# Kernel tuning notes

Measured on AMD Instinct MI355X. Metric: run time of the kernel, lower is better.

Reference implementation:

```python
import jax, jax.numpy as jnp
import numpy as np
from jax import lax

# Production-scale RPN detection-head config
B, FH, FW, NA = 8, 200, 200, 9      # batch, fmap h, fmap w, anchors/cell
H, W = 800, 800                      # image dims
N = FH * FW * NA                     # 360k anchors per image
NMS_THR = 0.7
MIN_SIZE = 1e-3


def _make_anchors():
    scales = np.array([32.0, 64.0, 128.0])
    ratios = np.array([0.5, 1.0, 2.0])
    ws = (scales[:, None] * np.sqrt(1.0 / ratios)[None, :]).reshape(-1)  # [NA]
    hs = (scales[:, None] * np.sqrt(ratios)[None, :]).reshape(-1)
    sy, sx = H / FH, W / FW
    cx = (np.arange(FW) + 0.5) * sx
    cy = (np.arange(FH) + 0.5) * sy
    cxg, cyg = np.meshgrid(cx, cy)                     # [FH,FW]
    cxg = cxg[..., None]; cyg = cyg[..., None]         # [FH,FW,1]
    a = np.stack([cxg - ws / 2, cyg - hs / 2, cxg + ws / 2, cyg + hs / 2], axis=-1)
    return jnp.asarray(a.reshape(-1, 4), jnp.float32)  # [N,4] xyxy


def setup_inputs() -> dict:
    key = jax.random.key(0)
    k1, k2 = jax.random.split(key)
    cls_logits = jax.random.normal(k1, (B, N, 1), jnp.float32)
    reg_deltas = jax.random.normal(k2, (B, N, 4), jnp.float32) * 0.1  # sane exp(dw)
    anchors = jnp.broadcast_to(_make_anchors()[None], (B, N, 4))
    return {
        "cls_logits": cls_logits,
        "reg_deltas": reg_deltas,
        "anchors": anchors,
        "keep_pre_nms": 1000,
        "keep_post_nms": 300,
    }


def _offsets2boxes(deltas, anchors):
    aw = anchors[:, 2] - anchors[:, 0]
    ah = anchors[:, 3] - anchors[:, 1]
    acx = anchors[:, 0] + 0.5 * aw
    acy = anchors[:, 1] + 0.5 * ah
    cx = deltas[:, 0] * aw + acx
    cy = deltas[:, 1] * ah + acy
    w = jnp.exp(deltas[:, 2]) * aw
    h = jnp.exp(deltas[:, 3]) * ah
    return jnp.stack([cx - 0.5 * w, cy - 0.5 * h, cx + 0.5 * w, cy + 0.5 * h], axis=-1)


def _iou_matrix(b):
    area = (b[:, 2] - b[:, 0]) * (b[:, 3] - b[:, 1])
    lt = jnp.maximum(b[:, None, :2], b[None, :, :2])
    rb = jnp.minimum(b[:, None, 2:], b[None, :, 2:])
    wh = jnp.clip(rb - lt, 0.0)
    inter = wh[..., 0] * wh[..., 1]
    return inter / (area[:, None] + area[None, :] - inter + 1e-9)


def _detect_one(logit, delta, anc, pre, post):
    scores = jax.nn.sigmoid(logit.reshape(-1))             # [N]
    boxes = _offsets2boxes(delta.reshape(-1, 4), anc)      # [N,4]
    s, idx = lax.top_k(scores, pre)                        # sorted desc
    b = boxes[idx]                                         # [pre,4]
    # clip to image
    b = jnp.stack([
        jnp.clip(b[:, 0], 0.0, W), jnp.clip(b[:, 1], 0.0, H),
        jnp.clip(b[:, 2], 0.0, W), jnp.clip(b[:, 3], 0.0, H)], axis=-1)
    valid = ((b[:, 2] - b[:, 0]) >= MIN_SIZE) & ((b[:, 3] - b[:, 1]) >= MIN_SIZE)
    # greedy NMS on score-sorted boxes (mask-based, fixed shapes)
    iou = _iou_matrix(lax.stop_gradient(b))                # [pre,pre]
    j = jnp.arange(pre)

    def body(keep, i):
        sup = (iou[i] > NMS_THR) & (j > i) & keep[i]
        return keep & ~sup, None

    keep, _ = lax.scan(body, valid, jnp.arange(pre))
    # compact first `post` kept detections into fixed [post,5], zero-padded
    dets = jnp.concatenate([b, s[:, None]], axis=-1)       # [pre,5]
    rank = jnp.cumsum(keep) - 1
    tgt = jnp.where(keep & (rank < post), rank, post)
    out = jnp.zeros((post + 1, 5), dets.dtype).at[tgt].set(dets)[:post]
    return out


def reference(cls_logits, reg_deltas, anchors, keep_pre_nms, keep_post_nms):
    f = lambda l, d, a: _detect_one(l, d, a, keep_pre_nms, keep_post_nms)
    return jax.vmap(f)(cls_logits, reg_deltas, anchors)    # [B,post,5]
```

## Files before the change

### kernel.cpp

```cpp
#include <hip/hip_runtime.h>
#include <stdint.h>
#include <math.h>

typedef unsigned long long u64;
typedef unsigned int u32;

#define NPI   360000
#define B_IMG 8
#define PRE   1000
#define POST  300
#define CAP   4096
#define NMSF  0.7f
#define IMG_W 800.0f
#define IMG_H 800.0f

#define NBIN    4096
#define KSHIFT  20
#define NGRP    64
#define CHUNK_H 30
#define F4PB_H  (NPI / 4 / CHUNK_H)
#define CHUNK_C 48
#define F4PB_C  (NPI / 4 / CHUNK_C)
#define EPB_C   (NPI / CHUNK_C)
#define LBUF    1024

#define CNT_OFF     0
#define VALID_OFF   256
#define PHIST_OFF   4096
#define PCOARSE_OFF 3936256
#define BOX_OFF     3997696
#define SCORE_OFF   4125696
#define CAND_OFF    4157696
#define MASK_OFF    4419840

#define LDSROWS 496
#define NMS_T   320

__device__ __forceinline__ u32 fkey(float f) {
  u32 u = __float_as_uint(f);
  return (u & 0x80000000u) ? ~u : (u | 0x80000000u);
}
__device__ __forceinline__ u64 rl64(u64 v, int lane) {
  u32 lo = (u32)__builtin_amdgcn_readlane((int)(u32)v, lane);
  u32 hi = (u32)__builtin_amdgcn_readlane((int)(u32)(v >> 32), lane);
  return ((u64)hi << 32) | lo;
}
__device__ __forceinline__ u64 sx64(u64 v, int m) {
  u32 lo = (u32)__shfl_xor((int)(u32)v, m, 64);
  u32 hi = (u32)__shfl_xor((int)(u32)(v >> 32), m, 64);
  return ((u64)hi << 32) | lo;
}

__global__ __launch_bounds__(256) void k_hist(const float* __restrict__ logits,
                                              u32* __restrict__ phist,
                                              u32* __restrict__ pcoarse,
                                              u32* __restrict__ cnt,
                                              u64* __restrict__ validw) {
  __shared__ u32 h[NBIN];
  const int img = blockIdx.y, c = blockIdx.x;
  const int tid = threadIdx.x;
  for (int i = tid; i < NBIN; i += 256) h[i] = 0;
  __syncthreads();
  const float4* L = (const float4*)(logits + (size_t)img * NPI) + (size_t)c * F4PB_H;
  for (int i = tid; i < F4PB_H; i += 256) {
    float4 v = L[i];
    atomicAdd(&h[fkey(v.x) >> KSHIFT], 1u);
    atomicAdd(&h[fkey(v.y) >> KSHIFT], 1u);
    atomicAdd(&h[fkey(v.z) >> KSHIFT], 1u);
    atomicAdd(&h[fkey(v.w) >> KSHIFT], 1u);
  }
  __syncthreads();
  u32* P = phist + ((size_t)img * CHUNK_H + c) * NBIN;
  for (int i = tid; i < NBIN; i += 256) P[i] = h[i];
  if (tid < NGRP) {
    u32 s = 0;
#pragma unroll
    for (int b = 0; b < NBIN / NGRP; b++) s += h[tid * (NBIN / NGRP) + b];
    pcoarse[((size_t)img * CHUNK_H + c) * NGRP + tid] = s;
  }
  if (c == 0) {
    if (tid < 16) validw[img * 16 + tid] = 0;
    if (img == 0 && tid < B_IMG) cnt[tid] = 0;
  }
}

__global__ __launch_bounds__(256) void k_compact(const float* __restrict__ logits,
                                                 const u32* __restrict__ phist,
                                                 const u32* __restrict__ pcoarse,
                                                 u32* __restrict__ cnt,
                                                 u64* __restrict__ cand) {
  __shared__ u64 buf[LBUF];
  __shared__ u32 bcnt;
  __shared__ u32 gbase;
  __shared__ int stb;
  const int img = blockIdx.y, c = blockIdx.x;
  const int t = threadIdx.x;
  if (t == 0) { bcnt = 0; stb = 0; }
  if (t < 64) {
    const u32* PC = pcoarse + (size_t)img * CHUNK_H * NGRP;
    u32 cg = 0;
    for (int cc = 0; cc < CHUNK_H; cc++) cg += PC[cc * NGRP + t];
    u32 suf = cg;
#pragma unroll
    for (int off = 1; off < 64; off <<= 1) {
      u32 o = (u32)__shfl_down((int)suf, off, 64);
      if (t + off < 64) suf += o;
    }
    u32 sx = suf - cg;
    u64 bal = __ballot(suf >= (u32)PRE && sx < (u32)PRE);
    if (bal) {
      int gc = __builtin_ctzll(bal);
      u32 s_above = (u32)__shfl((int)sx, gc, 64);
      const u32* P = phist + (size_t)img * CHUNK_H * NBIN + gc * (NBIN / NGRP);
      u32 fb = 0;
      for (int cc = 0; cc < CHUNK_H; cc++) fb += P[(size_t)cc * NBIN + t];
      u32 fsuf = fb;
#pragma unroll
      for (int off = 1; off < 64; off <<= 1) {
        u32 o = (u32)__shfl_down((int)fsuf, off, 64);
        if (t + off < 64) fsuf += o;
      }
      u32 fincl = fsuf + s_above;
      u32 fexcl = fincl - fb;
      if (fincl >= (u32)PRE && fexcl < (u32)PRE) stb = gc * (NBIN / NGRP) + t;
    }
  }
  __syncthreads();
  const int tb = stb;
  const float4* L = (const float4*)(logits + (size_t)img * NPI) + (size_t)c * F4PB_C;
  const int ebase = c * EPB_C;
  for (int i = t; i < F4PB_C; i += 256) {
    float4 v = L[i];
    float xs[4] = {v.x, v.y, v.z, v.w};
#pragma unroll
    for (int q = 0; q < 4; q++) {
      float x = xs[q];
      if ((int)(fkey(x) >> KSHIFT) >= tb) {
        float ef = (float)exp(-(double)x);
        float sg = 1.0f / (1.0f + ef);
        u32 e = (u32)(ebase + 4 * i + q);
        u32 p = atomicAdd(&bcnt, 1u);
        if (p < LBUF)
          buf[p] = ((u64)fkey(sg) << 32) | (u64)(0xFFFFFFFFu - e);
      }
    }
  }
  __syncthreads();
  if (t == 0) {
    u32 m = bcnt < LBUF ? bcnt : LBUF;
    bcnt = m;
    gbase = atomicAdd(&cnt[img], m);
  }
  __syncthreads();
  const u32 m = bcnt, gb = gbase;
  for (u32 j = t; j < m; j += 256) {
    u32 pos = gb + j;
    if (pos < CAP) cand[img * CAP + pos] = buf[j];
  }
}

__device__ __forceinline__ void emit_row(
    int img, int row, u64 key,
    const float* __restrict__ deltas, const float* __restrict__ anchors,
    float4* __restrict__ boxes, float* __restrict__ scores, u64* __restrict__ validw) {
  u32 hi  = (u32)(key >> 32);
  u32 idx = 0xFFFFFFFFu - (u32)(key & 0xFFFFFFFFu);
  u32 su  = (hi & 0x80000000u) ? (hi ^ 0x80000000u) : ~hi;
  float sc = __uint_as_float(su);
  size_t off = (size_t)img * NPI + idx;
  float4 d = ((const float4*)deltas)[off];
  float4 a = ((const float4*)anchors)[off];
  float aw = a.z - a.x, ah = a.w - a.y;
  float acx = a.x + 0.5f * aw, acy = a.y + 0.5f * ah;
  float cx = d.x * aw + acx, cy = d.y * ah + acy;
  float w = expf(d.z) * aw, h = expf(d.w) * ah;
  float x1 = cx - 0.5f * w, y1 = cy - 0.5f * h;
  float x2 = cx + 0.5f * w, y2 = cy + 0.5f * h;
  x1 = fminf(fmaxf(x1, 0.f), IMG_W);
  y1 = fminf(fmaxf(y1, 0.f), IMG_H);
  x2 = fminf(fmaxf(x2, 0.f), IMG_W);
  y2 = fminf(fmaxf(y2, 0.f), IMG_H);
  boxes[img * PRE + row]  = make_float4(x1, y1, x2, y2);
  scores[img * PRE + row] = sc;
  if (((x2 - x1) >= 1e-3f) && ((y2 - y1) >= 1e-3f))
    atomicOr(&validw[img * 16 + (row >> 6)], 1ull << (row & 63));
}

#define RB 8
__global__ __launch_bounds__(256) void k_rank(
    const float* __restrict__ deltas, const float* __restrict__ anchors,
    const u32* __restrict__ cnt, const u64* __restrict__ cand,
    float4* __restrict__ boxes, float* __restrict__ scores, u64* __restrict__ validw) {
  __shared__ u64 skey[CAP];
  const int img = blockIdx.y;
  int n = (int)cnt[img];
  if (n > CAP) n = CAP;
  for (int i = threadIdx.x; i < n; i += 256) skey[i] = cand[img * CAP + i];
  __syncthreads();
  const int r0 = blockIdx.x * 256 + threadIdx.x;
  const int r1 = r0 + RB * 256;
  u64 k0 = (r0 < n) ? skey[r0] : 0ull;
  u64 k1 = (r1 < n) ? skey[r1] : 0ull;
  int c0 = 0, c1 = 0;
  for (int j = 0; j < n; j++) {
    u64 kj = skey[j];
    c0 += (kj > k0);
    c1 += (kj > k1);
  }
  if (r0 < n && c0 < PRE) emit_row(img, c0, k0, deltas, anchors, boxes, scores, validw);
  if (r1 < n && c1 < PRE) emit_row(img, c1, k1, deltas, anchors, boxes, scores, validw);
}

__global__ __launch_bounds__(1024) void k_iou(const float4* __restrict__ boxes,
                                              u64* __restrict__ mask) {
  __shared__ float4 sb[1024];
  __shared__ float  sa[1024];
  const int img = blockIdx.y;
  const int tid = threadIdx.x;
  {
    float4 b = (tid < PRE) ? boxes[img * PRE + tid]
                           : make_float4(0.f, 0.f, 0.f, 0.f);
    sb[tid] = b;
    sa[tid] = (b.z - b.x) * (b.w - b.y);
  }
  __syncthreads();
  const int lane = tid & 63;
  const int wv   = tid >> 6;
  const int i    = blockIdx.x * 64 + lane;
  const bool rowok = (i < PRE);
  const float4 bi = sb[blockIdx.x * 64 + lane];
  const float  ai = sa[blockIdx.x * 64 + lane];
  const int cbase = wv << 6;
  u64 bits = 0;
#pragma unroll
  for (int k = 0; k < 64; k++) {
    int c = cbase + k;
    float4 bc = sb[c];
    float ac  = sa[c];
    float ltx = fmaxf(bi.x, bc.x), lty = fmaxf(bi.y, bc.y);
    float rbx = fminf(bi.z, bc.z), rby = fminf(bi.w, bc.w);
    float iw = fmaxf(rbx - ltx, 0.f), ih = fmaxf(rby - lty, 0.f);
    float inter = iw * ih;
    float iou = inter / (ai + ac - inter + 1e-9f);
    bits |= (iou > NMSF) ? (1ull << k) : 0ull;
  }
  int d = i - cbase;
  u64 gtmask = (d < 0) ? ~0ull : ((d >= 63) ? 0ull : (~0ull << (d + 1)));
  int rem = PRE - cbase;
  u64 tmask = (rem >= 64) ? ~0ull : ((rem <= 0) ? 0ull : ((1ull << rem) - 1ull));
  bits &= gtmask & tmask;
  if (rowok) mask[((size_t)img * PRE + i) * 16 + wv] = bits;
}

__global__ __launch_bounds__(NMS_T) void k_nms(
    const u64* __restrict__ mask, const u64* __restrict__ validw,
    const float4* __restrict__ boxes, const float* __restrict__ scores,
    float* __restrict__ out) {
  __shared__ u64 smask[LDSROWS * 16];
  __shared__ int skeeplist[POST];
  __shared__ int skept;
  const int img = blockIdx.x;
  const int tid = threadIdx.x;
  const u64* M = mask + (size_t)img * PRE * 16;
  u64 diag[16];
  if (tid < 64) {
#pragma unroll
    for (int cc = 0; cc < 16; cc++) {
      int row = cc * 64 + tid;
      diag[cc] = (row < PRE) ? M[(size_t)row * 16 + cc] : 0ull;
    }
  }
  for (int e = tid; e < LDSROWS * 16; e += NMS_T) smask[e] = M[e];
  __syncthreads();
  if (tid < 64) {
    const int lane = tid;
    const int w = lane & 15, g = lane >> 4;
    u64 rem = ~0ull;
    if (lane < 16) {
      rem = ~validw[img * 16 + lane];
      if (lane == 15) rem |= 0xFFFFFF0000000000ull;
    }
    int kept = 0;
#pragma unroll
    for (int cc = 0; cc < 16; cc++) {
      u64 alive = ~rl64(rem, cc);
      int kept0 = kept;
      while (alive != 0ull && kept < POST) {
        int r = __builtin_ctzll(alive);
        if (lane == 0) skeeplist[kept] = cc * 64 + r;
        kept++;
        u64 sup = rl64(diag[cc], r);
        alive &= ~sup;
        alive &= ~(1ull << r);
      }
      int nc = kept - kept0;
      if (nc > 0 && kept < POST && cc < 15) {
        u64 part = 0;
        for (int j = g; j < nc; j += 4) {
          int row = skeeplist[kept0 + j];
          part |= (row < LDSROWS) ? smask[row * 16 + w] : M[(size_t)row * 16 + w];
        }
        part |= sx64(part, 16);
        part |= sx64(part, 32);
        rem |= part;
      }
      if (kept >= POST) break;
    }
    if (lane == 0) skept = kept;
  }
  __syncthreads();
  if (tid < POST) {
    float4 bx = make_float4(0.f, 0.f, 0.f, 0.f);
    float  sc = 0.f;
    if (tid < skept) {
      int i = skeeplist[tid];
      bx = boxes[img * PRE + i];
      sc = scores[img * PRE + i];
    }
    float* o = out + ((size_t)img * POST + tid) * 5;
    o[0] = bx.x; o[1] = bx.y; o[2] = bx.z; o[3] = bx.w; o[4] = sc;
  }
}

extern "C" void kernel_launch(void* const* d_in, const int* in_sizes, int n_in,
                              void* d_out, int out_size, void* d_ws, size_t ws_size,
                              hipStream_t stream) {
  const float* logits  = (const float*)d_in[0];
  const float* deltas  = (const float*)d_in[1];
  const float* anchors = (const float*)d_in[2];
  float* out = (float*)d_out;
  char* ws = (char*)d_ws;

  u32* cnt      = (u32*)(ws + CNT_OFF);
  u64* validw   = (u64*)(ws + VALID_OFF);
  u32* phist    = (u32*)(ws + PHIST_OFF);
  u32* pcoarse  = (u32*)(ws + PCOARSE_OFF);
  float4* boxes = (float4*)(ws + BOX_OFF);
  float* scores = (float*)(ws + SCORE_OFF);
  u64* cand     = (u64*)(ws + CAND_OFF);
  u64* mask     = (u64*)(ws + MASK_OFF);

  dim3 gh(CHUNK_H, B_IMG);
  k_hist<<<gh, 256, 0, stream>>>(logits, phist, pcoarse, cnt, validw);
  dim3 gc(CHUNK_C, B_IMG);
  k_compact<<<gc, 256, 0, stream>>>(logits, phist, pcoarse, cnt, cand);
  dim3 gr(RB, B_IMG);
  k_rank<<<gr, 256, 0, stream>>>(deltas, anchors, cnt, cand, boxes, scores, validw);
  dim3 g2(16, B_IMG);
  k_iou<<<g2, 1024, 0, stream>>>(boxes, mask);
  k_nms<<<B_IMG, NMS_T, 0, stream>>>(mask, validw, boxes, scores, out);
}
```

Before: 207.1 us.

## Split histogram bins, prefetch logits in compact, parallelize rank counting across waves

The histogram kernel uses four sub-histograms chosen by thread group to cut LDS atomic contention, then reduces them and computes coarse sums with wave shuffles. The compact kernel issues its logit loads into registers before the threshold search so the memory latency overlaps the prefix scan. The rank kernel runs 16 blocks with an early exit. Each wave counts over a quarter of the candidates for 256 rows, and the partial counts are summed in LDS. This raises parallelism in what was a serial O(n) loop per thread. The cost is more LDS and registers, which may lower occupancy.

```diff
diff --git a/kernel.cpp b/kernel.cpp
--- a/kernel.cpp
+++ b/kernel.cpp
@@ -35,6 +35,7 @@
 
 #define LDSROWS 496
 #define NMS_T   320
+#define RBLK    16
 
 __device__ __forceinline__ u32 fkey(float f) {
   u32 u = __float_as_uint(f);
@@ -56,27 +57,33 @@
                                               u32* __restrict__ pcoarse,
                                               u32* __restrict__ cnt,
                                               u64* __restrict__ validw) {
-  __shared__ u32 h[NBIN];
+  __shared__ u32 h[4 * NBIN];
   const int img = blockIdx.y, c = blockIdx.x;
   const int tid = threadIdx.x;
-  for (int i = tid; i < NBIN; i += 256) h[i] = 0;
-  __syncthreads();
+  for (int i = tid; i < 4 * NBIN; i += 256) h[i] = 0;
+  __syncthreads();
+  const int salt = ((tid >> 4) & 3) * NBIN;
   const float4* L = (const float4*)(logits + (size_t)img * NPI) + (size_t)c * F4PB_H;
   for (int i = tid; i < F4PB_H; i += 256) {
     float4 v = L[i];
-    atomicAdd(&h[fkey(v.x) >> KSHIFT], 1u);
-    atomicAdd(&h[fkey(v.y) >> KSHIFT], 1u);
-    atomicAdd(&h[fkey(v.z) >> KSHIFT], 1u);
-    atomicAdd(&h[fkey(v.w) >> KSHIFT], 1u);
+    atomicAdd(&h[salt + (fkey(v.x) >> KSHIFT)], 1u);
+    atomicAdd(&h[salt + (fkey(v.y) >> KSHIFT)], 1u);
+    atomicAdd(&h[salt + (fkey(v.z) >> KSHIFT)], 1u);
+    atomicAdd(&h[salt + (fkey(v.w) >> KSHIFT)], 1u);
   }
   __syncthreads();
   u32* P = phist + ((size_t)img * CHUNK_H + c) * NBIN;
-  for (int i = tid; i < NBIN; i += 256) P[i] = h[i];
-  if (tid < NGRP) {
-    u32 s = 0;
-#pragma unroll
-    for (int b = 0; b < NBIN / NGRP; b++) s += h[tid * (NBIN / NGRP) + b];
-    pcoarse[((size_t)img * CHUNK_H + c) * NGRP + tid] = s;
+  u32* PC = pcoarse + ((size_t)img * CHUNK_H + c) * NGRP;
+  const int lane = tid & 63;
+#pragma unroll
+  for (int k = 0; k < NBIN / 256; k++) {
+    int i = k * 256 + tid;
+    u32 v = h[i] + h[NBIN + i] + h[2 * NBIN + i] + h[3 * NBIN + i];
+    P[i] = v;
+    u32 s = v;
+#pragma unroll
+    for (int m = 1; m < 64; m <<= 1) s += (u32)__shfl_xor((int)s, m, 64);
+    if (lane == 0) PC[i >> 6] = s;
   }
   if (c == 0) {
     if (tid < 16) validw[img * 16 + tid] = 0;
@@ -96,6 +103,13 @@
   const int img = blockIdx.y, c = blockIdx.x;
   const int t = threadIdx.x;
   if (t == 0) { bcnt = 0; stb = 0; }
+  const float4* L = (const float4*)(logits + (size_t)img * NPI) + (size_t)c * F4PB_C;
+  float4 r[8];
+#pragma unroll
+  for (int k = 0; k < 8; k++) {
+    int i = t + k * 256;
+    if (i < F4PB_C) r[k] = L[i];
+  }
   if (t < 64) {
     const u32* PC = pcoarse + (size_t)img * CHUNK_H * NGRP;
     u32 cg = 0;
@@ -127,21 +141,23 @@
   }
   __syncthreads();
   const int tb = stb;
-  const float4* L = (const float4*)(logits + (size_t)img * NPI) + (size_t)c * F4PB_C;
   const int ebase = c * EPB_C;
-  for (int i = t; i < F4PB_C; i += 256) {
-    float4 v = L[i];
-    float xs[4] = {v.x, v.y, v.z, v.w};
-#pragma unroll
-    for (int q = 0; q < 4; q++) {
-      float x = xs[q];
-      if ((int)(fkey(x) >> KSHIFT) >= tb) {
-        float ef = (float)exp(-(double)x);
-        float sg = 1.0f / (1.0f + ef);
-        u32 e = (u32)(ebase + 4 * i + q);
-        u32 p = atomicAdd(&bcnt, 1u);
-        if (p < LBUF)
-          buf[p] = ((u64)fkey(sg) << 32) | (u64)(0xFFFFFFFFu - e);
+#pragma unroll
+  for (int k = 0; k < 8; k++) {
+    int i = t + k * 256;
+    if (i < F4PB_C) {
+      float xs[4] = {r[k].x, r[k].y, r[k].z, r[k].w};
+#pragma unroll
+      for (int q = 0; q < 4; q++) {
+        float x = xs[q];
+        if ((int)(fkey(x) >> KSHIFT) >= tb) {
+          float ef = (float)exp(-(double)x);
+          float sg = 1.0f / (1.0f + ef);
+          u32 e = (u32)(ebase + 4 * i + q);
+          u32 p = atomicAdd(&bcnt, 1u);
+          if (p < LBUF)
+            buf[p] = ((u64)fkey(sg) << 32) | (u64)(0xFFFFFFFFu - e);
+        }
       }
     }
   }
@@ -186,29 +202,42 @@
     atomicOr(&validw[img * 16 + (row >> 6)], 1ull << (row & 63));
 }
 
-#define RB 8
 __global__ __launch_bounds__(256) void k_rank(
     const float* __restrict__ deltas, const float* __restrict__ anchors,
     const u32* __restrict__ cnt, const u64* __restrict__ cand,
     float4* __restrict__ boxes, float* __restrict__ scores, u64* __restrict__ validw) {
   __shared__ u64 skey[CAP];
+  __shared__ u32 pc[4][256];
   const int img = blockIdx.y;
   int n = (int)cnt[img];
   if (n > CAP) n = CAP;
+  const int base = blockIdx.x * 256;
+  if (base >= n) return;
   for (int i = threadIdx.x; i < n; i += 256) skey[i] = cand[img * CAP + i];
   __syncthreads();
-  const int r0 = blockIdx.x * 256 + threadIdx.x;
-  const int r1 = r0 + RB * 256;
+  const int w = threadIdx.x >> 6, l = threadIdx.x & 63;
+  const int r0 = base + l, r1 = r0 + 64, r2 = r0 + 128, r3 = r0 + 192;
   u64 k0 = (r0 < n) ? skey[r0] : 0ull;
   u64 k1 = (r1 < n) ? skey[r1] : 0ull;
-  int c0 = 0, c1 = 0;
-  for (int j = 0; j < n; j++) {
+  u64 k2 = (r2 < n) ? skey[r2] : 0ull;
+  u64 k3 = (r3 < n) ? skey[r3] : 0ull;
+  int c0 = 0, c1 = 0, c2 = 0, c3 = 0;
+  const int js = (w * n) >> 2, je = ((w + 1) * n) >> 2;
+  for (int j = js; j < je; j++) {
     u64 kj = skey[j];
-    c0 += (kj > k0);
-    c1 += (kj > k1);
-  }
-  if (r0 < n && c0 < PRE) emit_row(img, c0, k0, deltas, anchors, boxes, scores, validw);
-  if (r1 < n && c1 < PRE) emit_row(img, c1, k1, deltas, anchors, boxes, scores, validw);
+    c0 += (kj > k0); c1 += (kj > k1); c2 += (kj > k2); c3 += (kj > k3);
+  }
+  pc[w][l]       = (u32)c0;
+  pc[w][l + 64]  = (u32)c1;
+  pc[w][l + 128] = (u32)c2;
+  pc[w][l + 192] = (u32)c3;
+  __syncthreads();
+  const int t = threadIdx.x;
+  const int rr = base + t;
+  if (rr < n) {
+    int c = (int)(pc[0][t] + pc[1][t] + pc[2][t] + pc[3][t]);
+    if (c < PRE) emit_row(img, c, skey[rr], deltas, anchors, boxes, scores, validw);
+  }
 }
 
 __global__ __launch_bounds__(1024) void k_iou(const float4* __restrict__ boxes,
@@ -344,7 +373,7 @@
   k_hist<<<gh, 256, 0, stream>>>(logits, phist, pcoarse, cnt, validw);
   dim3 gc(CHUNK_C, B_IMG);
   k_compact<<<gc, 256, 0, stream>>>(logits, phist, pcoarse, cnt, cand);
-  dim3 gr(RB, B_IMG);
+  dim3 gr(RBLK, B_IMG);
   k_rank<<<gr, 256, 0, stream>>>(deltas, anchors, cnt, cand, boxes, scores, validw);
   dim3 g2(16, B_IMG);
   k_iou<<<g2, 1024, 0, stream>>>(boxes, mask);
```

New measurement: 210.2 us. No clear change (+1.5%).
